# Kernel optimization log

Measured on AMD Instinct MI355X. Metric: run time of the kernel, lower is better.

## Reference

```python
import jax, jax.numpy as jnp
import numpy as np

DIM, HID, BATCH = 64, 512, 8192


def setup_inputs() -> dict:
    key = jax.random.key(0)
    ks = jax.random.split(key, 6)
    s1 = 1.0 / np.sqrt(DIM + 1)
    s2 = 1.0 / np.sqrt(HID)
    return {
        "t": jax.random.uniform(ks[0], (1,), dtype=jnp.float32),
        "x": jax.random.normal(ks[1], (BATCH, DIM), dtype=jnp.float32),
        "W1": jax.random.normal(ks[2], (DIM + 1, HID), dtype=jnp.float32) * s1,
        "b1": jnp.zeros((HID,), jnp.float32),
        "W2": jax.random.normal(ks[3], (HID, HID), dtype=jnp.float32) * s2,
        "b2": jnp.zeros((HID,), jnp.float32),
        "W3": jax.random.normal(ks[4], (HID, DIM), dtype=jnp.float32) * s2,
        "b3": jnp.zeros((DIM,), jnp.float32),
    }


def _vf_single(ts, xs, W1, b1, W2, b2, W3, b3):
    # xs: [dim], ts: scalar. Time concatenated as extra input feature.
    h = jnp.concatenate([xs, ts[None]])          # [dim+1]
    h = jnp.tanh(h @ W1 + b1)                    # [hid]
    h = jnp.tanh(h @ W2 + b2)                    # [hid]
    return h @ W3 + b3                           # [dim]


def reference(t, x, W1, b1, W2, b2, W3, b3):
    ts = t[0]
    vf = lambda xs: _vf_single(ts, xs, W1, b1, W2, b2, W3, b3)
    v = jax.vmap(vf)(x)                                   # [B, dim]
    # Exact divergence: trace of per-sample Jacobian dv/dx.
    # (Replaces the torch per-dim autograd.grad loop with one batched jacfwd.)
    J = jax.vmap(jax.jacfwd(vf))(x)                       # [B, dim, dim]
    div = jnp.trace(J, axis1=-2, axis2=-1)                # [B]
    return (v, -div[:, None])
```

## Files before the change

kernel.cpp:

```cpp
#include <hip/hip_runtime.h>

#define DIM 64
#define HID 512
#define BATCH 8192
#define MB 32
#define NTHR 1024

typedef __attribute__((ext_vector_type(8))) short short8;
typedef __attribute__((ext_vector_type(4))) float f32x4;
typedef __attribute__((ext_vector_type(16))) float f32x16;
typedef float float4_ __attribute__((ext_vector_type(4)));
typedef unsigned long long ull;

#define Z16 {0.f,0.f,0.f,0.f,0.f,0.f,0.f,0.f,0.f,0.f,0.f,0.f,0.f,0.f,0.f,0.f}

union U8 { short8 s8; unsigned short u[8]; };
union U4 { ull v; unsigned short u[4]; };
union FB { unsigned u; float f; };

__device__ __forceinline__ unsigned short f2bf(float f) {
    union { float f; unsigned u; } v; v.f = f;
    return (unsigned short)((v.u + 0x7FFFu + ((v.u >> 16) & 1u)) >> 16);
}
__device__ __forceinline__ float bf2f(unsigned short b) {
    FB v; v.u = (unsigned)b << 16; return v.f;
}
__device__ __forceinline__ float tanh_fast(float x) {
    float e = __expf(2.f * x);
    return 1.f - __fdividef(2.f, e + 1.f);
}

__global__ __launch_bounds__(256) void prep(
        const float* __restrict__ t,  const float* __restrict__ W1,
        const float* __restrict__ b1, const float* __restrict__ W2,
        const float* __restrict__ W3,
        unsigned short* __restrict__ w2pk, unsigned short* __restrict__ ppk,
        unsigned short* __restrict__ w3pk, unsigned short* __restrict__ w1pk,
        float* __restrict__ c1) {
    __shared__ float w3sT[DIM * 33];
    __shared__ float w1s[DIM * DIM];
    int b = blockIdx.x;
    if (b >= 288) {
        int n = (b - 288) * 256 + threadIdx.x;
        c1[n] = fmaf(t[0], W1[DIM * HID + n], b1[n]);
        return;
    }
    int gid = b * 256 + threadIdx.x;
    int f = gid >> 6, l = gid & 63;
    if (f < 512) {
        int nt = f >> 5, ks = f & 31;
        int n = nt * 32 + (l & 31), k0 = ks * 16 + (l >> 5) * 8;
        unsigned short* o = w2pk + (size_t)(f * 64 + l) * 8;
#pragma unroll
        for (int e = 0; e < 8; ++e) o[e] = f2bf(W2[(size_t)(k0 + e) * HID + n]);
    } else if (f < 1024) {
        int ntb = (b * 4 - 512) >> 5;
        int jb  = (((b - 128) * 4) & 31) * 16;
        for (int idx = threadIdx.x; idx < 32 * DIM; idx += 256) {
            int dn = idx >> 6, i = idx & 63;
            w3sT[i * 33 + dn] = W3[(size_t)(ntb * 32 + dn) * DIM + i];
        }
        for (int idx = threadIdx.x; idx < DIM * DIM; idx += 256) {
            int i = idx >> 6, jj = idx & 63;
            w1s[i * DIM + jj] = W1[(size_t)i * HID + jb + jj];
        }
        __syncthreads();
        int fi = f - 512;
        int ks = fi & 31;
        int dn = l & 31, k0 = ks * 16 + (l >> 5) * 8;
        int n = ntb * 32 + dn;
        int jo = k0 - jb;
        float m[8] = {0.f,0.f,0.f,0.f,0.f,0.f,0.f,0.f};
#pragma unroll
        for (int i = 0; i < DIM; ++i) {
            float w3 = w3sT[i * 33 + dn];
            const float* wrow = &w1s[i * DIM + jo];
#pragma unroll
            for (int e = 0; e < 8; ++e) m[e] = fmaf(wrow[e], w3, m[e]);
        }
        unsigned short* o = ppk + (size_t)(fi * 64 + l) * 8;
#pragma unroll
        for (int e = 0; e < 8; ++e) o[e] = f2bf(W2[(size_t)(k0 + e) * HID + n] * m[e]);
    } else if (f < 1088) {
        int fi = f - 1024;
        int nt = fi >> 4, ks = fi & 15;
        int n = nt * 16 + (l & 15), k0 = ks * 32 + (l >> 4) * 8;
        unsigned short* o = w3pk + (size_t)(fi * 64 + l) * 8;
#pragma unroll
        for (int e = 0; e < 8; ++e) o[e] = f2bf(W3[(size_t)(k0 + e) * DIM + n]);
    } else {
        int fi = f - 1088;
        int nt = fi >> 1, ks = fi & 1;
        int n = nt * 16 + (l & 15), k0 = ks * 32 + (l >> 4) * 8;
        unsigned short* o = w1pk + (size_t)(fi * 64 + l) * 8;
#pragma unroll
        for (int e = 0; e < 8; ++e) o[e] = f2bf(W1[(size_t)(k0 + e) * HID + n]);
    }
}

__device__ __forceinline__ int act_addr(int sample, int colbyte) {
    return (sample * 1024 + colbyte) ^ ((sample & 15) << 4);
}

__global__ __launch_bounds__(NTHR)
__attribute__((amdgpu_waves_per_eu(4, 4)))
void fused_main(
        const float* __restrict__ x,  const float* __restrict__ c1,
        const float* __restrict__ b2, const float* __restrict__ b3,
        const unsigned short* __restrict__ w1pk, const unsigned short* __restrict__ w2pk,
        const unsigned short* __restrict__ ppk,  const unsigned short* __restrict__ w3pk,
        float* __restrict__ out) {
    __shared__ unsigned short h1s[MB * HID];
    __shared__ unsigned short d1s[MB * HID];
    __shared__ unsigned short h2s[MB * HID];
    __shared__ float wred[8][MB];
    char* h1b = (char*)h1s; char* d1b = (char*)d1s; char* h2b = (char*)h2s;

    const int tid = threadIdx.x, w = tid >> 6, l = tid & 63;
    const int lr = l & 15, g = l >> 4;
    const int s0 = blockIdx.x * MB;

    short8 xf[2][2];
#pragma unroll
    for (int nt = 0; nt < 2; ++nt)
#pragma unroll
        for (int ks = 0; ks < 2; ++ks) {
            const float* xp = x + (size_t)(s0 + nt * 16 + lr) * DIM + ks * 32 + g * 8;
            float4_ x0 = *(const float4_*)xp;
            float4_ x1 = *(const float4_*)(xp + 4);
            U8 u;
            u.u[0]=f2bf(x0.x); u.u[1]=f2bf(x0.y); u.u[2]=f2bf(x0.z); u.u[3]=f2bf(x0.w);
            u.u[4]=f2bf(x1.x); u.u[5]=f2bf(x1.y); u.u[6]=f2bf(x1.z); u.u[7]=f2bf(x1.w);
            xf[nt][ks] = u.s8;
        }
#pragma unroll
    for (int mi = 0; mi < 2; ++mi) {
        int mt = w * 2 + mi;
        short8 a0 = ((const short8*)w1pk)[(size_t)((mt * 2 + 0) * 64 + l)];
        short8 a1 = ((const short8*)w1pk)[(size_t)((mt * 2 + 1) * 64 + l)];
        float c1q[4];
#pragma unroll
        for (int r = 0; r < 4; ++r) c1q[r] = c1[mt * 16 + g * 4 + r];
#pragma unroll
        for (int nt = 0; nt < 2; ++nt) {
            f32x4 acc = {0.f, 0.f, 0.f, 0.f};
            acc = __builtin_amdgcn_mfma_f32_16x16x32_bf16(a0, xf[nt][0], acc, 0, 0, 0);
            acc = __builtin_amdgcn_mfma_f32_16x16x32_bf16(a1, xf[nt][1], acc, 0, 0, 0);
            int sample = nt * 16 + lr;
            U4 hu, du;
#pragma unroll
            for (int r = 0; r < 4; ++r) {
                float h = tanh_fast(acc[r] + c1q[r]);
                hu.u[r] = f2bf(h);
                du.u[r] = f2bf(fmaf(-h, h, 1.f));
            }
            int ab = act_addr(sample, (mt * 16 + g * 4) * 2);
            *(ull*)(h1b + ab) = hu.v;
            *(ull*)(d1b + ab) = du.v;
        }
    }
    __syncthreads();

    const int q = w & 7, role = w >> 3;
    const short8* Bf = (const short8*)(role ? ppk : w2pk);
    const char* Ab = role ? d1b : h1b;
    const short8* b0p = Bf + (size_t)((2 * q + 0) * 32) * 64 + l;
    const short8* b1p = Bf + (size_t)((2 * q + 1) * 32) * 64 + l;
    f32x16 a0 = Z16, a1 = Z16;
#pragma unroll 4
    for (int ks = 0; ks < 32; ++ks) {
        int ab = act_addr(l & 31, ks * 32 + (l >> 5) * 16);
        short8 av  = *(const short8*)(Ab + ab);
        short8 b0v = b0p[ks * 64];
        short8 b1v = b1p[ks * 64];
        a0 = __builtin_amdgcn_mfma_f32_32x32x16_bf16(av, b0v, a0, 0, 0, 0);
        a1 = __builtin_amdgcn_mfma_f32_32x32x16_bf16(av, b1v, a1, 0, 0, 0);
    }

    if (role == 0) {
#pragma unroll
        for (int j = 0; j < 2; ++j) {
            int c = (2 * q + j) * 32 + (l & 31);
            float b2v = b2[c];
            f32x16 acc = j ? a1 : a0;
#pragma unroll
            for (int r = 0; r < 16; ++r) {
                int row = (r & 3) + 8 * (r >> 2) + 4 * (l >> 5);
                float h2 = tanh_fast(acc[r] + b2v);
                *(unsigned short*)(h2b + act_addr(row, c * 2)) = f2bf(h2);
            }
        }
    }
    __syncthreads();

    if (role == 1) {
        float divp[16];
#pragma unroll
        for (int r = 0; r < 16; ++r) divp[r] = 0.f;
#pragma unroll
        for (int j = 0; j < 2; ++j) {
            int c = (2 * q + j) * 32 + (l & 31);
            f32x16 acc = j ? a1 : a0;
#pragma unroll
            for (int r = 0; r < 16; ++r) {
                int row = (r & 3) + 8 * (r >> 2) + 4 * (l >> 5);
                float h2 = bf2f(*(const unsigned short*)(h2b + act_addr(row, c * 2)));
                divp[r] = fmaf(acc[r], fmaf(-h2, h2, 1.f), divp[r]);
            }
        }
#pragma unroll
        for (int off = 1; off < 32; off <<= 1) {
#pragma unroll
            for (int r = 0; r < 16; ++r) divp[r] += __shfl_xor(divp[r], off, 64);
        }
        if ((l & 31) == 0) {
#pragma unroll
            for (int r = 0; r < 16; ++r) {
                int row = (r & 3) + 8 * (r >> 2) + 4 * (l >> 5);
                wred[q][row] = divp[r];
            }
        }
    } else {
        const int wm3 = w & 1, wn3 = w >> 1;
        f32x4 acc = {0.f, 0.f, 0.f, 0.f};
        const short8* W3f = (const short8*)w3pk + (size_t)(wn3 * 16) * 64 + l;
#pragma unroll
        for (int ks = 0; ks < 16; ++ks) {
            int ab = act_addr(wm3 * 16 + lr, ks * 64 + g * 16);
            short8 ah = *(const short8*)(h2b + ab);
            acc = __builtin_amdgcn_mfma_f32_16x16x32_bf16(ah, W3f[ks * 64], acc, 0, 0, 0);
        }
        int c = wn3 * 16 + lr;
        float b3v = b3[c];
#pragma unroll
        for (int r = 0; r < 4; ++r)
            out[(size_t)(s0 + wm3 * 16 + g * 4 + r) * DIM + c] = acc[r] + b3v;
    }
    __syncthreads();
    if (tid < MB) {
        float d = 0.f;
#pragma unroll
        for (int ww = 0; ww < 8; ++ww) d += wred[ww][tid];
        out[(size_t)BATCH * DIM + s0 + tid] = -d;
    }
}

extern "C" void kernel_launch(void* const* d_in, const int* in_sizes, int n_in,
                              void* d_out, int out_size, void* d_ws, size_t ws_size,
                              hipStream_t stream) {
    const float* t  = (const float*)d_in[0];
    const float* x  = (const float*)d_in[1];
    const float* W1 = (const float*)d_in[2];
    const float* b1 = (const float*)d_in[3];
    const float* W2 = (const float*)d_in[4];
    const float* b2 = (const float*)d_in[5];
    const float* W3 = (const float*)d_in[6];
    const float* b3 = (const float*)d_in[7];
    float* out = (float*)d_out;

    char* ws = (char*)d_ws;
    unsigned short* w2pk = (unsigned short*)ws;
    unsigned short* ppk  = (unsigned short*)(ws + (512 << 10));
    unsigned short* w3pk = (unsigned short*)(ws + (1 << 20));
    unsigned short* w1pk = (unsigned short*)(ws + (1 << 20) + (64 << 10));
    float*          c1   = (float*)(ws + (1 << 20) + (128 << 10));

    prep<<<290, 256, 0, stream>>>(t, W1, b1, W2, W3, w2pk, ppk, w3pk, w1pk, c1);
    fused_main<<<BATCH / MB, NTHR, 0, stream>>>(x, c1, b2, b3, w1pk, w2pk, ppk, w3pk, out);
}
```

Measured before the change: 33.20 us.

## Double-buffer W2/P weight fragments into LDS via async global_load_lds

The second-layer weight fragments are now streamed with global_load_lds into a per-wave double-buffered LDS staging area, which is reused as the h2 buffer afterwards. Manual vmcnt and lgkmcnt waits plus sched barriers keep two k-steps of loads in flight while the MFMAs run. The aim is to hide global load latency in the main GEMM loop without raising register pressure, and the overlapping h2 storage saves LDS. The cost is an extra __syncthreads and full unrolling of the loop, and the correctness of the hand-written wait counts depends on the compiler emitting no other vector memory ops inside the loop.

```diff
diff --git a/kernel.cpp b/kernel.cpp
--- a/kernel.cpp
+++ b/kernel.cpp
@@ -28,6 +28,11 @@
 __device__ __forceinline__ float tanh_fast(float x) {
     float e = __expf(2.f * x);
     return 1.f - __fdividef(2.f, e + 1.f);
+}
+__device__ __forceinline__ void gl_lds16(const void* g, void* l) {
+    __builtin_amdgcn_global_load_lds(
+        (const __attribute__((address_space(1))) unsigned*)g,
+        (__attribute__((address_space(3))) unsigned*)l, 16, 0, 0);
 }
 
 __global__ __launch_bounds__(256) void prep(
@@ -112,9 +117,10 @@
         float* __restrict__ out) {
     __shared__ unsigned short h1s[MB * HID];
     __shared__ unsigned short d1s[MB * HID];
-    __shared__ unsigned short h2s[MB * HID];
+    __shared__ unsigned short stage[2 * 16 * 2 * 512];
     __shared__ float wred[8][MB];
-    char* h1b = (char*)h1s; char* d1b = (char*)d1s; char* h2b = (char*)h2s;
+    char* h1b = (char*)h1s; char* d1b = (char*)d1s;
+    char* stageb = (char*)stage; char* h2b = (char*)stage;
 
     const int tid = threadIdx.x, w = tid >> 6, l = tid & 63;
     const int lr = l & 15, g = l >> 4;
@@ -162,20 +168,37 @@
     __syncthreads();
 
     const int q = w & 7, role = w >> 3;
-    const short8* Bf = (const short8*)(role ? ppk : w2pk);
+    const char* Bf = (const char*)(role ? ppk : w2pk);
     const char* Ab = role ? d1b : h1b;
-    const short8* b0p = Bf + (size_t)((2 * q + 0) * 32) * 64 + l;
-    const short8* b1p = Bf + (size_t)((2 * q + 1) * 32) * 64 + l;
+#define SLOT(buf, j) (stageb + (((buf) * 16 + w) * 2 + (j)) * 1024)
+#define ISSUE(buf, ks)                                                          \
+    {                                                                           \
+        gl_lds16(Bf + ((size_t)((2 * q + 0) * 32 + (ks)) * 64 + l) * 16, SLOT(buf, 0)); \
+        gl_lds16(Bf + ((size_t)((2 * q + 1) * 32 + (ks)) * 64 + l) * 16, SLOT(buf, 1)); \
+    }
+    ISSUE(0, 0)
+    ISSUE(1, 1)
     f32x16 a0 = Z16, a1 = Z16;
-#pragma unroll 4
+#pragma unroll
     for (int ks = 0; ks < 32; ++ks) {
-        int ab = act_addr(l & 31, ks * 32 + (l >> 5) * 16);
-        short8 av  = *(const short8*)(Ab + ab);
-        short8 b0v = b0p[ks * 64];
-        short8 b1v = b1p[ks * 64];
+        const int buf = ks & 1;
+        if (ks == 31) { asm volatile("s_waitcnt vmcnt(0)" ::: "memory"); }
+        else          { asm volatile("s_waitcnt vmcnt(2)" ::: "memory"); }
+        __builtin_amdgcn_sched_barrier(0);
+        short8 b0v = *(const short8*)(SLOT(buf, 0) + l * 16);
+        short8 b1v = *(const short8*)(SLOT(buf, 1) + l * 16);
+        short8 av  = *(const short8*)(Ab + act_addr(l & 31, ks * 32 + (l >> 5) * 16));
         a0 = __builtin_amdgcn_mfma_f32_32x32x16_bf16(av, b0v, a0, 0, 0, 0);
         a1 = __builtin_amdgcn_mfma_f32_32x32x16_bf16(av, b1v, a1, 0, 0, 0);
-    }
+        if (ks + 2 < 32) {
+            asm volatile("s_waitcnt lgkmcnt(0)" ::: "memory");
+            __builtin_amdgcn_sched_barrier(0);
+            ISSUE(buf, ks + 2)
+        }
+    }
+#undef ISSUE
+#undef SLOT
+    __syncthreads();
 
     if (role == 0) {
 #pragma unroll
@@ -186,8 +209,7 @@
 #pragma unroll
             for (int r = 0; r < 16; ++r) {
                 int row = (r & 3) + 8 * (r >> 2) + 4 * (l >> 5);
-                float h2 = tanh_fast(acc[r] + b2v);
-                *(unsigned short*)(h2b + act_addr(row, c * 2)) = f2bf(h2);
+                *(unsigned short*)(h2b + act_addr(row, c * 2)) = f2bf(tanh_fast(acc[r] + b2v));
             }
         }
     }
@@ -226,8 +248,7 @@
         const short8* W3f = (const short8*)w3pk + (size_t)(wn3 * 16) * 64 + l;
 #pragma unroll
         for (int ks = 0; ks < 16; ++ks) {
-            int ab = act_addr(wm3 * 16 + lr, ks * 64 + g * 16);
-            short8 ah = *(const short8*)(h2b + ab);
+            short8 ah = *(const short8*)(h2b + act_addr(wm3 * 16 + lr, ks * 64 + g * 16));
             acc = __builtin_amdgcn_mfma_f32_16x16x32_bf16(ah, W3f[ks * 64], acc, 0, 0, 0);
         }
         int c = wn3 * 16 + lr;
```

Result: slower. 35.28 us (+6.2%).
